# Optimization experiments

Hardware: AMD Instinct MI355X
Metric: run time of the kernel (lower is better)

The kernel has to match this reference:

```python
import jax, jax.numpy as jnp
import numpy as np
import math

B, H, S, DK, DV = 4, 16, 2048, 128, 128


def setup_inputs() -> dict:
    key = jax.random.key(0)
    kq, kk, kv = jax.random.split(key, 3)
    Q = jax.random.normal(kq, (B, H, S, DK), dtype=jnp.float32)
    K = jax.random.normal(kk, (B, H, S, DK), dtype=jnp.float32)
    V = jax.random.normal(kv, (B, H, S, DV), dtype=jnp.float32)
    # causal mask: True = attend
    mask = jnp.tril(jnp.ones((S, S), dtype=bool))
    return {"Q": Q, "K": K, "V": V, "mask": mask}


def reference(Q, K, V, mask):
    d_k = K.shape[-1]
    # [B,H,Sq,Skv] scores
    scores = jnp.einsum("bhqd,bhkd->bhqk", Q, K) / math.sqrt(d_k)
    scores = jnp.where(mask, scores, -jnp.inf)
    attn = jax.nn.softmax(scores, axis=-1)  # stable: subtract rowmax, exp, normalize
    return jnp.einsum("bhqk,bhkv->bhqv", attn, V)
```

## Files before the change

### kernel.cpp

```cpp
#include <hip/hip_runtime.h>
#include <hip/hip_bf16.h>


#define S_LEN 2048
#define DKC   128
#define DVC   128
#define BM    128
#define BN    64
#define KPAD  136
#define VPAD  72
#define PPAD  72

typedef __bf16 bf16;
typedef bf16  bf16x4 __attribute__((ext_vector_type(4)));
typedef bf16  bf16x8 __attribute__((ext_vector_type(8)));
typedef float f32x4  __attribute__((ext_vector_type(4)));

__global__ __launch_bounds__(256, 2)
void fa_kernel(const float* __restrict__ Q, const float* __restrict__ K,
               const float* __restrict__ V, float* __restrict__ O) {
  __shared__ bf16 Klds[2][BN][KPAD];
  __shared__ bf16 Vlds[DVC][VPAD];
  __shared__ bf16 Plds[4][32][PPAD];

  const int tid  = threadIdx.x;
  const int w    = tid >> 6;
  const int lane = tid & 63;
  const int quad = lane >> 4;
  const int l16  = lane & 15;

  const int lin = blockIdx.x;
  const int xcd = lin & 7;
  const int idx = lin >> 3;
  const int qt  = 15 - (idx & 15);
  const int bh  = xcd + 8 * (idx >> 4);

  const int q0 = qt * BM;
  const size_t base = (size_t)bh * S_LEN * DKC;
  const float* Qp = Q + base;
  const float* Kp = K + base;
  const float* Vp = V + base;
  float*       Op = O + base;

  const float SCALE2 = 0.08838834764831845f * 1.4426950408889634f;

  bf16x8 qf[2][4];
#pragma unroll
  for (int g = 0; g < 2; ++g) {
    const float* qrow = Qp + (size_t)(q0 + w * 32 + g * 16 + l16) * DKC;
#pragma unroll
    for (int c = 0; c < 4; ++c) {
      const float* p = qrow + c * 32 + quad * 8;
      float4 x = *(const float4*)p;
      float4 y = *(const float4*)(p + 4);
      bf16x8 f;
      f[0] = (bf16)(x.x * SCALE2); f[1] = (bf16)(x.y * SCALE2);
      f[2] = (bf16)(x.z * SCALE2); f[3] = (bf16)(x.w * SCALE2);
      f[4] = (bf16)(y.x * SCALE2); f[5] = (bf16)(y.y * SCALE2);
      f[6] = (bf16)(y.z * SCALE2); f[7] = (bf16)(y.w * SCALE2);
      qf[g][c] = f;
    }
  }

  f32x4 oacc[2][8];
#pragma unroll
  for (int g = 0; g < 2; ++g)
#pragma unroll
    for (int n = 0; n < 8; ++n)
#pragma unroll
      for (int r = 0; r < 4; ++r) oacc[g][n][r] = 0.0f;
  float lrow[2][4] = {{0.f, 0.f, 0.f, 0.f}, {0.f, 0.f, 0.f, 0.f}};

  const int krow = tid >> 5;
  const int kcol = (tid & 31) * 4;
  const int vk   = tid & 31;
  const int vd   = tid >> 5;

  const int ntiles = 2 * qt + 2;

  float4 kx[8], vx[8];
#pragma unroll
  for (int i = 0; i < 8; ++i)
    kx[i] = *(const float4*)(Kp + (size_t)(krow + i * 8) * DKC + kcol);
#pragma unroll
  for (int i = 0; i < 8; ++i) {
    int k  = vk + 32 * (i & 1);
    int d4 = (vd + 8 * (i >> 1)) * 4;
    vx[i] = *(const float4*)(Vp + (size_t)k * DVC + d4);
  }

  for (int t = 0; t < ntiles; ++t) {
    const int buf = t & 1;
    const int kvb = t * BN;

#pragma unroll
    for (int i = 0; i < 8; ++i) {
      bf16x4 k4;
      k4[0] = (bf16)kx[i].x; k4[1] = (bf16)kx[i].y;
      k4[2] = (bf16)kx[i].z; k4[3] = (bf16)kx[i].w;
      *(bf16x4*)&Klds[buf][krow + i * 8][kcol] = k4;
    }
    if (t + 1 < ntiles) {
      const int kvb2 = kvb + BN;
#pragma unroll
      for (int i = 0; i < 8; ++i)
        kx[i] = *(const float4*)(Kp + (size_t)(kvb2 + krow + i * 8) * DKC + kcol);
    }
    asm volatile("s_waitcnt lgkmcnt(0)\n\ts_barrier" ::: "memory");

#pragma unroll
    for (int i = 0; i < 8; ++i) {
      int k  = vk + 32 * (i & 1);
      int d4 = (vd + 8 * (i >> 1)) * 4;
      Vlds[d4 + 0][k] = (bf16)vx[i].x;
      Vlds[d4 + 1][k] = (bf16)vx[i].y;
      Vlds[d4 + 2][k] = (bf16)vx[i].z;
      Vlds[d4 + 3][k] = (bf16)vx[i].w;
    }
    asm volatile("s_waitcnt lgkmcnt(0)\n\ts_barrier" ::: "memory");

    if (t + 1 < ntiles) {
      const int kvb2 = kvb + BN;
#pragma unroll
      for (int i = 0; i < 8; ++i) {
        int k  = vk + 32 * (i & 1);
        int d4 = (vd + 8 * (i >> 1)) * 4;
        vx[i] = *(const float4*)(Vp + (size_t)(kvb2 + k) * DVC + d4);
      }
    }

    f32x4 sacc[2][4];
#pragma unroll
    for (int g = 0; g < 2; ++g)
#pragma unroll
      for (int n = 0; n < 4; ++n)
#pragma unroll
        for (int r = 0; r < 4; ++r) sacc[g][n][r] = 0.0f;
#pragma unroll
    for (int c = 0; c < 4; ++c) {
#pragma unroll
      for (int n = 0; n < 4; ++n) {
        bf16x8 kf = *(const bf16x8*)&Klds[buf][n * 16 + l16][c * 32 + quad * 8];
        sacc[0][n] = __builtin_amdgcn_mfma_f32_16x16x32_bf16(qf[0][c], kf, sacc[0][n], 0, 0, 0);
        sacc[1][n] = __builtin_amdgcn_mfma_f32_16x16x32_bf16(qf[1][c], kf, sacc[1][n], 0, 0, 0);
      }
    }

    if (t >= ntiles - 2) {
#pragma unroll
      for (int g = 0; g < 2; ++g)
#pragma unroll
        for (int n = 0; n < 4; ++n) {
          int kg = kvb + n * 16 + l16;
#pragma unroll
          for (int r = 0; r < 4; ++r) {
            int qg = q0 + w * 32 + g * 16 + quad * 4 + r;
            if (kg > qg) sacc[g][n][r] = -1e30f;
          }
        }
    }

#pragma unroll
    for (int g = 0; g < 2; ++g)
#pragma unroll
      for (int r = 0; r < 4; ++r) {
        float ps = 0.0f;
#pragma unroll
        for (int n = 0; n < 4; ++n) {
          float p = exp2f(sacc[g][n][r]);
          sacc[g][n][r] = p;
          ps += p;
        }
        lrow[g][r] += ps;
      }

#pragma unroll
    for (int g = 0; g < 2; ++g)
#pragma unroll
      for (int n = 0; n < 4; ++n)
#pragma unroll
        for (int r = 0; r < 4; ++r)
          Plds[w][g * 16 + quad * 4 + r][n * 16 + l16] = (bf16)sacc[g][n][r];

#pragma unroll
    for (int c = 0; c < 2; ++c) {
      bf16x8 pf0 = *(const bf16x8*)&Plds[w][l16][c * 32 + quad * 8];
      bf16x8 pf1 = *(const bf16x8*)&Plds[w][16 + l16][c * 32 + quad * 8];
#pragma unroll
      for (int n = 0; n < 8; ++n) {
        bf16x8 vf = *(const bf16x8*)&Vlds[n * 16 + l16][c * 32 + quad * 8];
        oacc[0][n] = __builtin_amdgcn_mfma_f32_16x16x32_bf16(pf0, vf, oacc[0][n], 0, 0, 0);
        oacc[1][n] = __builtin_amdgcn_mfma_f32_16x16x32_bf16(pf1, vf, oacc[1][n], 0, 0, 0);
      }
    }
  }

#pragma unroll
  for (int g = 0; g < 2; ++g) {
    float linv[4];
#pragma unroll
    for (int r = 0; r < 4; ++r) {
      float s = lrow[g][r];
      s += __shfl_xor(s, 1);
      s += __shfl_xor(s, 2);
      s += __shfl_xor(s, 4);
      s += __shfl_xor(s, 8);
      linv[r] = 1.0f / s;
    }
#pragma unroll
    for (int n = 0; n < 8; ++n) {
#pragma unroll
      for (int r = 0; r < 4; ++r) {
        int qg = q0 + w * 32 + g * 16 + quad * 4 + r;
        Op[(size_t)qg * DVC + n * 16 + l16] = oacc[g][n][r] * linv[r];
      }
    }
  }
}

extern "C" void kernel_launch(void* const* d_in, const int* in_sizes, int n_in,
                              void* d_out, int out_size, void* d_ws, size_t ws_size,
                              hipStream_t stream) {
  const float* Q = (const float*)d_in[0];
  const float* K = (const float*)d_in[1];
  const float* V = (const float*)d_in[2];
  float* O = (float*)d_out;
  dim3 grid(1024);
  fa_kernel<<<grid, 256, 0, stream>>>(Q, K, V, O);
}
```

Baseline: 368.4 us.

## Keep P in registers via transposed QK^T and permlane swaps instead of LDS

Computes S transposed (K as the A operand) so each lane holds four consecutive key scores for one query row. It then packs exp2 results to bf16 with v_cvt_pk_bf16_f32 and rearranges them with v_permlane32/16_swap into the PV MFMA operand layout. This removes the per-wave Plds shared-memory round trip, and the row-sum reduction becomes a per-lane sum plus cross-quad shuffles. The gain is less LDS traffic and fewer waits, at the cost of relying on gfx950-specific permlane instructions and a correct lane mapping.

```diff
diff --git a/kernel.cpp b/kernel.cpp
--- a/kernel.cpp
+++ b/kernel.cpp
@@ -9,19 +9,19 @@
 #define BN    64
 #define KPAD  136
 #define VPAD  72
-#define PPAD  72
 
 typedef __bf16 bf16;
 typedef bf16  bf16x4 __attribute__((ext_vector_type(4)));
 typedef bf16  bf16x8 __attribute__((ext_vector_type(8)));
 typedef float f32x4  __attribute__((ext_vector_type(4)));
+typedef unsigned int u32;
+typedef u32 u32x4 __attribute__((ext_vector_type(4)));
 
 __global__ __launch_bounds__(256, 2)
 void fa_kernel(const float* __restrict__ Q, const float* __restrict__ K,
                const float* __restrict__ V, float* __restrict__ O) {
   __shared__ bf16 Klds[2][BN][KPAD];
   __shared__ bf16 Vlds[DVC][VPAD];
-  __shared__ bf16 Plds[4][32][PPAD];
 
   const int tid  = threadIdx.x;
   const int w    = tid >> 6;
@@ -50,9 +50,9 @@
     const float* qrow = Qp + (size_t)(q0 + w * 32 + g * 16 + l16) * DKC;
 #pragma unroll
     for (int c = 0; c < 4; ++c) {
-      const float* p = qrow + c * 32 + quad * 8;
-      float4 x = *(const float4*)p;
-      float4 y = *(const float4*)(p + 4);
+      const float* pq = qrow + c * 32 + quad * 8;
+      float4 x = *(const float4*)pq;
+      float4 y = *(const float4*)(pq + 4);
       bf16x8 f;
       f[0] = (bf16)(x.x * SCALE2); f[1] = (bf16)(x.y * SCALE2);
       f[2] = (bf16)(x.z * SCALE2); f[3] = (bf16)(x.w * SCALE2);
@@ -69,7 +69,7 @@
     for (int n = 0; n < 8; ++n)
 #pragma unroll
       for (int r = 0; r < 4; ++r) oacc[g][n][r] = 0.0f;
-  float lrow[2][4] = {{0.f, 0.f, 0.f, 0.f}, {0.f, 0.f, 0.f, 0.f}};
+  float lsum[2] = {0.0f, 0.0f};
 
   const int krow = tid >> 5;
   const int kcol = (tid & 31) * 4;
@@ -129,84 +129,76 @@
       }
     }
 
-    f32x4 sacc[2][4];
-#pragma unroll
-    for (int g = 0; g < 2; ++g)
-#pragma unroll
-      for (int n = 0; n < 4; ++n)
-#pragma unroll
-        for (int r = 0; r < 4; ++r) sacc[g][n][r] = 0.0f;
-#pragma unroll
-    for (int c = 0; c < 4; ++c) {
-#pragma unroll
-      for (int n = 0; n < 4; ++n) {
+    u32 W[2][4][2];
+#pragma unroll
+    for (int n = 0; n < 4; ++n) {
+      f32x4 sacc[2];
+#pragma unroll
+      for (int g = 0; g < 2; ++g)
+#pragma unroll
+        for (int r = 0; r < 4; ++r) sacc[g][r] = 0.0f;
+#pragma unroll
+      for (int c = 0; c < 4; ++c) {
         bf16x8 kf = *(const bf16x8*)&Klds[buf][n * 16 + l16][c * 32 + quad * 8];
-        sacc[0][n] = __builtin_amdgcn_mfma_f32_16x16x32_bf16(qf[0][c], kf, sacc[0][n], 0, 0, 0);
-        sacc[1][n] = __builtin_amdgcn_mfma_f32_16x16x32_bf16(qf[1][c], kf, sacc[1][n], 0, 0, 0);
-      }
-    }
-
-    if (t >= ntiles - 2) {
-#pragma unroll
-      for (int g = 0; g < 2; ++g)
-#pragma unroll
-        for (int n = 0; n < 4; ++n) {
-          int kg = kvb + n * 16 + l16;
-#pragma unroll
-          for (int r = 0; r < 4; ++r) {
-            int qg = q0 + w * 32 + g * 16 + quad * 4 + r;
-            if (kg > qg) sacc[g][n][r] = -1e30f;
-          }
+        sacc[0] = __builtin_amdgcn_mfma_f32_16x16x32_bf16(kf, qf[0][c], sacc[0], 0, 0, 0);
+        sacc[1] = __builtin_amdgcn_mfma_f32_16x16x32_bf16(kf, qf[1][c], sacc[1], 0, 0, 0);
+      }
+      if (t >= ntiles - 2) {
+        const int kg = kvb + n * 16 + quad * 4;
+#pragma unroll
+        for (int g = 0; g < 2; ++g) {
+          const int qg = q0 + w * 32 + g * 16 + l16;
+#pragma unroll
+          for (int r = 0; r < 4; ++r)
+            if (kg + r > qg) sacc[g][r] = -1e30f;
         }
-    }
-
-#pragma unroll
-    for (int g = 0; g < 2; ++g)
-#pragma unroll
-      for (int r = 0; r < 4; ++r) {
-        float ps = 0.0f;
-#pragma unroll
-        for (int n = 0; n < 4; ++n) {
-          float p = exp2f(sacc[g][n][r]);
-          sacc[g][n][r] = p;
-          ps += p;
+      }
+#pragma unroll
+      for (int g = 0; g < 2; ++g) {
+        float p0 = exp2f(sacc[g][0]);
+        float p1 = exp2f(sacc[g][1]);
+        float p2 = exp2f(sacc[g][2]);
+        float p3 = exp2f(sacc[g][3]);
+        lsum[g] += (p0 + p1) + (p2 + p3);
+        asm("v_cvt_pk_bf16_f32 %0, %1, %2" : "=v"(W[g][n][0]) : "v"(p0), "v"(p1));
+        asm("v_cvt_pk_bf16_f32 %0, %1, %2" : "=v"(W[g][n][1]) : "v"(p2), "v"(p3));
+      }
+    }
+
+#pragma unroll
+    for (int c = 0; c < 2; ++c) {
+      bf16x8 pf[2];
+#pragma unroll
+      for (int g = 0; g < 2; ++g) {
+        u32x4 pw;
+#pragma unroll
+        for (int h = 0; h < 2; ++h) {
+          u32 pa = W[g][2 * c][h], pb = W[g][2 * c + 1][h];
+          asm("v_permlane32_swap_b32 %0, %1" : "+v"(pa), "+v"(pb));
+          asm("v_permlane16_swap_b32 %0, %1" : "+v"(pa), "+v"(pb));
+          pw[h]     = pa;
+          pw[2 + h] = pb;
         }
-        lrow[g][r] += ps;
-      }
-
-#pragma unroll
-    for (int g = 0; g < 2; ++g)
-#pragma unroll
-      for (int n = 0; n < 4; ++n)
-#pragma unroll
-        for (int r = 0; r < 4; ++r)
-          Plds[w][g * 16 + quad * 4 + r][n * 16 + l16] = (bf16)sacc[g][n][r];
-
-#pragma unroll
-    for (int c = 0; c < 2; ++c) {
-      bf16x8 pf0 = *(const bf16x8*)&Plds[w][l16][c * 32 + quad * 8];
-      bf16x8 pf1 = *(const bf16x8*)&Plds[w][16 + l16][c * 32 + quad * 8];
+        pf[g] = __builtin_bit_cast(bf16x8, pw);
+      }
 #pragma unroll
       for (int n = 0; n < 8; ++n) {
         bf16x8 vf = *(const bf16x8*)&Vlds[n * 16 + l16][c * 32 + quad * 8];
-        oacc[0][n] = __builtin_amdgcn_mfma_f32_16x16x32_bf16(pf0, vf, oacc[0][n], 0, 0, 0);
-        oacc[1][n] = __builtin_amdgcn_mfma_f32_16x16x32_bf16(pf1, vf, oacc[1][n], 0, 0, 0);
+        oacc[0][n] = __builtin_amdgcn_mfma_f32_16x16x32_bf16(pf[0], vf, oacc[0][n], 0, 0, 0);
+        oacc[1][n] = __builtin_amdgcn_mfma_f32_16x16x32_bf16(pf[1], vf, oacc[1][n], 0, 0, 0);
       }
     }
   }
 
 #pragma unroll
   for (int g = 0; g < 2; ++g) {
+    float s = lsum[g];
+    s += __shfl_xor(s, 16);
+    s += __shfl_xor(s, 32);
     float linv[4];
 #pragma unroll
-    for (int r = 0; r < 4; ++r) {
-      float s = lrow[g][r];
-      s += __shfl_xor(s, 1);
-      s += __shfl_xor(s, 2);
-      s += __shfl_xor(s, 4);
-      s += __shfl_xor(s, 8);
-      linv[r] = 1.0f / s;
-    }
+    for (int r = 0; r < 4; ++r)
+      linv[r] = 1.0f / __shfl(s, quad * 4 + r);
 #pragma unroll
     for (int n = 0; n < 8; ++n) {
 #pragma unroll
```

New measurement: 345.2 us. 6.3% less time.
